# Optimization experiments

Hardware: AMD Instinct MI355X
Metric: run time of the kernel (lower is better)

Reference implementation:

```python
import jax, jax.numpy as jnp
import numpy as np

N, E, H, L, B = 200000, 800000, 128, 4, 2000  # nodes, directed edges, hidden, layers, graphs
ATOM, BOND = 28, 6


def setup_inputs() -> dict:
    key = jax.random.key(0)
    ks = jax.random.split(key, 12)
    h = jax.random.normal(ks[0], (N, ATOM), jnp.float32)
    e = jax.random.normal(ks[1], (E, BOND), jnp.float32)
    # paired directed edges: edge 2i = (u->v), edge 2i+1 = (v->u), so rev(k) = k ^ 1
    u = jax.random.randint(ks[2], (E // 2,), 0, N)
    v = jax.random.randint(ks[3], (E // 2,), 0, N)
    src = jnp.stack([u, v], axis=1).reshape(-1)
    dst = jnp.stack([v, u], axis=1).reshape(-1)
    graph_id = jnp.sort(jax.random.randint(ks[4], (N,), 0, B))
    s = 1.0 / np.sqrt(H).astype(np.float32)
    W_emb = jax.random.normal(ks[5], (ATOM, H), jnp.float32) * (1.0 / np.sqrt(ATOM))
    W_init = jax.random.normal(ks[6], (H + BOND, H), jnp.float32) * s
    b_init = jnp.zeros((H,), jnp.float32)
    W_layers = jax.random.normal(ks[7], (L, H, H), jnp.float32) * s
    b_layers = jnp.zeros((L, H), jnp.float32)
    W_ro = jax.random.normal(ks[8], (H, H), jnp.float32) * s
    W_pred = jax.random.normal(ks[9], (H, 1), jnp.float32) * s
    b_pred = jnp.zeros((1,), jnp.float32)
    snorm_n = jnp.ones((N, 1), jnp.float32)
    snorm_e = jnp.ones((E, 1), jnp.float32)
    return dict(h=h, e=e, W_emb=W_emb, W_init=W_init, b_init=b_init,
                W_layers=W_layers, b_layers=b_layers, W_ro=W_ro,
                W_pred=W_pred, b_pred=b_pred, src=src, dst=dst,
                graph_id=graph_id, snorm_n=snorm_n, snorm_e=snorm_e)


def reference(h, e, W_emb, W_init, b_init, W_layers, b_layers, W_ro,
              W_pred, b_pred, src, dst, graph_id, snorm_n, snorm_e):
    n_nodes = h.shape[0]
    n_edges = src.shape[0]
    rev = jnp.arange(n_edges) ^ 1  # paired reverse-edge index
    # node embedding (dropout is identity at p=0); x kept as residual input per source
    x = h @ W_emb  # [N, H]
    # init_message_func: per-edge relu(Linear(cat(h_src, e)))
    he = jax.nn.relu(jnp.concatenate([x[src], e], axis=1) @ W_init + b_init)  # [E, H]
    # D-MPNN layers: aggregate incoming edge states at src node, exclude reverse edge,
    # linear + relu (norms disabled in this config), outer residual add
    n_layers = W_layers.shape[0]
    for l in range(n_layers):
        agg = jax.ops.segment_sum(he, dst, num_segments=n_nodes)  # sum of edge states into each node
        m = agg[src] - he[rev]                                    # exclude reverse edge
        he = jax.nn.relu(m @ W_layers[l] + b_layers[l]) + he      # residual
    # update_all(copy_edge, sum): node state = sum of incoming edge states
    h_out = jax.ops.segment_sum(he, dst, num_segments=n_nodes)  # [N, H]
    h_ro = h_out @ W_ro                                          # linear_ro (no bias)
    # readout == 'sum': per-graph sum of node states
    hg = jax.ops.segment_sum(h_ro, graph_id, num_segments=B)     # [B, H]
    return hg @ W_pred + b_pred                                  # [B, 1]
```

## Files before the change

kernel.cpp:

```cpp
#include <hip/hip_runtime.h>
#include <hip/hip_bf16.h>

#define H 128
#define ATOM 28
#define BOND 6
#define NLAYERS 4
#define TE 32
#define LW 136
#define LKI 72
#define LE 40
typedef unsigned short US;
typedef unsigned int UI;
typedef short bf16x8 __attribute__((ext_vector_type(8)));
typedef float f32x4 __attribute__((ext_vector_type(4)));
#define MFMA(a,b,c) __builtin_amdgcn_mfma_f32_16x16x32_bf16((a),(b),(c),0,0,0)

__device__ __forceinline__ float bf2f(US u) {
    union { unsigned int i; float f; } v; v.i = ((unsigned int)u) << 16; return v.f;
}
__device__ __forceinline__ US f2bf(float f) {
    union { float f; unsigned int i; } v; v.f = f;
    unsigned int r = v.i + 0x7FFF + ((v.i >> 16) & 1);
    return (US)(r >> 16);
}
__device__ __forceinline__ float in_ld(const void* p, long long i, int bf) {
    return bf ? bf2f(((const US*)p)[i]) : ((const float*)p)[i];
}

__global__ void detect_kernel(const void* snorm, int* flag) {
    const US* u = (const US*)snorm;
    *flag = (u[0] == 0x3F80 && u[2] == 0x3F80) ? 1 : 0;
}

__global__ void fail_kernel(void* out, int nB, float val, const int* flag) {
    int i = blockIdx.x * 256 + threadIdx.x;
    if (i < nB) {
        if (*flag) ((US*)out)[i] = f2bf(val);
        else       ((float*)out)[i] = val;
    }
}

__global__ void build_wt(const void* __restrict__ W_emb, const void* __restrict__ W_init,
                         const int* __restrict__ flag, US* __restrict__ WtG) {
    int bf = *flag;
    int k = blockIdx.x;
    int c = threadIdx.x;
    float v = 0.f;
    if (k < ATOM) {
        for (int j = 0; j < H; ++j)
            v += in_ld(W_emb, k * H + j, bf) * in_ld(W_init, (long long)j * H + c, bf);
    }
    WtG[c * 64 + k] = f2bf(v);
}

__global__ void build_w2x(const void* __restrict__ W_init, const int* __restrict__ flag,
                          US* __restrict__ W2x) {
    int bf = *flag;
    int k = blockIdx.x;
    int c = threadIdx.x;
    float v = (k < BOND) ? in_ld(W_init, (long long)(H + k) * H + c, bf) : 0.f;
    W2x[c * 32 + k] = f2bf(v);
}

__global__ void build_wtL(const void* __restrict__ W_layers, const int* __restrict__ flag,
                          US* __restrict__ WtL) {
    int bf = *flag;
    int l = blockIdx.x >> 7, n = blockIdx.x & 127;
    int k = threadIdx.x;
    long long si = (long long)l * H * H + (long long)k * H + n;
    WtL[((long long)l * H + n) * H + k] = bf ? ((const US*)W_layers)[si]
                                             : f2bf(((const float*)W_layers)[si]);
}

__global__ void build_wp(const void* __restrict__ W_ro, const void* __restrict__ W_pred,
                         const int* __restrict__ flag, float* __restrict__ wp) {
    int bf = *flag;
    int c = threadIdx.x;
    float s = 0.f;
    for (int j = 0; j < H; ++j)
        s += in_ld(W_ro, (long long)c * H + j, bf) * in_ld(W_pred, j, bf);
    wp[c] = s;
}

__global__ void hist_kernel(const int* __restrict__ dst, int* __restrict__ cnt, int nE) {
    int k = blockIdx.x * 256 + threadIdx.x;
    if (k < nE) atomicAdd(&cnt[dst[k]], 1);
}

__global__ __launch_bounds__(256) void scan1(const int* __restrict__ cnt,
                                             int* __restrict__ rowptr,
                                             int* __restrict__ partials, int nN) {
    __shared__ int sd[256];
    int t = threadIdx.x;
    int base = blockIdx.x * 1024 + t * 4;
    int l0 = (base + 0 < nN) ? cnt[base + 0] : 0;
    int l1 = (base + 1 < nN) ? cnt[base + 1] : 0;
    int l2 = (base + 2 < nN) ? cnt[base + 2] : 0;
    int l3 = (base + 3 < nN) ? cnt[base + 3] : 0;
    int s = l0 + l1 + l2 + l3;
    sd[t] = s; __syncthreads();
    for (int off = 1; off < 256; off <<= 1) {
        int v = (t >= off) ? sd[t - off] : 0;
        __syncthreads();
        sd[t] += v;
        __syncthreads();
    }
    int excl = sd[t] - s;
    if (base + 0 < nN) rowptr[base + 0] = excl;
    if (base + 1 < nN) rowptr[base + 1] = excl + l0;
    if (base + 2 < nN) rowptr[base + 2] = excl + l0 + l1;
    if (base + 3 < nN) rowptr[base + 3] = excl + l0 + l1 + l2;
    if (t == 255) partials[blockIdx.x] = sd[255];
}

__global__ __launch_bounds__(256) void scan2(const int* __restrict__ partials,
                                             int* __restrict__ blockoff, int SB) {
    __shared__ int sd[256];
    int t = threadIdx.x;
    int v = (t < SB) ? partials[t] : 0;
    sd[t] = v; __syncthreads();
    for (int off = 1; off < 256; off <<= 1) {
        int x = (t >= off) ? sd[t - off] : 0;
        __syncthreads();
        sd[t] += x;
        __syncthreads();
    }
    blockoff[t] = sd[t] - v;
}

__global__ void scan3(int* __restrict__ rowptr, int* __restrict__ cursor,
                      const int* __restrict__ blockoff, int nN, int nE) {
    int i = blockIdx.x * 256 + threadIdx.x;
    if (i < nN) {
        int v = rowptr[i] + blockoff[i >> 10];
        rowptr[i] = v;
        cursor[i] = v;
    }
    if (i == 0) rowptr[nN] = nE;
}

__global__ void fill_kernel(const int* __restrict__ dst, int* __restrict__ cursor,
                            int* __restrict__ ein, int nE) {
    int k = blockIdx.x * 256 + threadIdx.x;
    if (k < nE) {
        int pos = atomicAdd(&cursor[dst[k]], 1);
        ein[pos] = k;
    }
}

__global__ __launch_bounds__(256) void agg_gather(
    const US* __restrict__ he, const int* __restrict__ rowptr,
    const int* __restrict__ ein, US* __restrict__ agg, int nN) {
    int n = blockIdx.x * 4 + (threadIdx.x >> 6);
    int lane = threadIdx.x & 63;
    if (n >= nN) return;
    const UI* heU = (const UI*)he;
    int s = rowptr[n], epos = rowptr[n + 1];
    float f0 = 0.f, f1 = 0.f;
    int idx = s;
    for (; idx + 4 <= epos; idx += 4) {
        int e0 = ein[idx], e1 = ein[idx + 1], e2 = ein[idx + 2], e3 = ein[idx + 3];
        UI u0 = heU[(long long)e0 * 64 + lane];
        UI u1 = heU[(long long)e1 * 64 + lane];
        UI u2 = heU[(long long)e2 * 64 + lane];
        UI u3 = heU[(long long)e3 * 64 + lane];
        f0 += bf2f((US)(u0 & 0xFFFF)) + bf2f((US)(u1 & 0xFFFF))
            + bf2f((US)(u2 & 0xFFFF)) + bf2f((US)(u3 & 0xFFFF));
        f1 += bf2f((US)(u0 >> 16)) + bf2f((US)(u1 >> 16))
            + bf2f((US)(u2 >> 16)) + bf2f((US)(u3 >> 16));
    }
    for (; idx < epos; ++idx) {
        UI u = heU[(long long)ein[idx] * 64 + lane];
        f0 += bf2f((US)(u & 0xFFFF));
        f1 += bf2f((US)(u >> 16));
    }
    ((UI*)agg)[(long long)n * 64 + lane] = (UI)f2bf(f0) | ((UI)f2bf(f1) << 16);
}

__global__ __launch_bounds__(256) void readout_dot(
    const US* __restrict__ he, const int* __restrict__ rowptr,
    const int* __restrict__ ein, const float* __restrict__ wp,
    const int* __restrict__ graph_id, float* __restrict__ hgS, int nN) {
    __shared__ float sv[4];
    __shared__ int sg[4];
    int wave = threadIdx.x >> 6, lane = threadIdx.x & 63;
    int n = blockIdx.x * 4 + wave;
    bool valid = n < nN;
    float w0 = wp[2 * lane], w1 = wp[2 * lane + 1];
    float v = 0.f;
    if (valid) {
        const UI* heU = (const UI*)he;
        int s = rowptr[n], epos = rowptr[n + 1];
        float f0 = 0.f, f1 = 0.f;
        int idx = s;
        for (; idx + 4 <= epos; idx += 4) {
            int e0 = ein[idx], e1 = ein[idx + 1], e2 = ein[idx + 2], e3 = ein[idx + 3];
            UI u0 = heU[(long long)e0 * 64 + lane];
            UI u1 = heU[(long long)e1 * 64 + lane];
            UI u2 = heU[(long long)e2 * 64 + lane];
            UI u3 = heU[(long long)e3 * 64 + lane];
            f0 += bf2f((US)(u0 & 0xFFFF)) + bf2f((US)(u1 & 0xFFFF))
                + bf2f((US)(u2 & 0xFFFF)) + bf2f((US)(u3 & 0xFFFF));
            f1 += bf2f((US)(u0 >> 16)) + bf2f((US)(u1 >> 16))
                + bf2f((US)(u2 >> 16)) + bf2f((US)(u3 >> 16));
        }
        for (; idx < epos; ++idx) {
            UI u = heU[(long long)ein[idx] * 64 + lane];
            f0 += bf2f((US)(u & 0xFFFF));
            f1 += bf2f((US)(u >> 16));
        }
        v = f0 * w0 + f1 * w1;
        #pragma unroll
        for (int off = 32; off > 0; off >>= 1) v += __shfl_down(v, off);
    }
    if (lane == 0) {
        sv[wave] = valid ? v : 0.f;
        sg[wave] = valid ? graph_id[n] : -1;
    }
    __syncthreads();
    if (threadIdx.x == 0) {
        int cg = sg[0]; float acc = sv[0];
        #pragma unroll
        for (int w = 1; w < 4; ++w) {
            if (sg[w] == cg) acc += sv[w];
            else {
                if (cg >= 0) unsafeAtomicAdd(&hgS[cg], acc);
                cg = sg[w]; acc = sv[w];
            }
        }
        if (cg >= 0) unsafeAtomicAdd(&hgS[cg], acc);
    }
}

__global__ __launch_bounds__(256) void agg_dot(
    const US* __restrict__ agg, const float* __restrict__ wp,
    const int* __restrict__ graph_id, float* __restrict__ hgS, int nN) {
    __shared__ float sv[4];
    __shared__ int sg[4];
    int wave = threadIdx.x >> 6, lane = threadIdx.x & 63;
    int n = blockIdx.x * 4 + wave;
    bool valid = n < nN;
    float v = 0.f;
    if (valid) {
        UI u = ((const UI*)agg)[(long long)n * 64 + lane];
        v = bf2f((US)(u & 0xFFFF)) * wp[2 * lane]
          + bf2f((US)(u >> 16)) * wp[2 * lane + 1];
        #pragma unroll
        for (int off = 32; off > 0; off >>= 1) v += __shfl_down(v, off);
    }
    if (lane == 0) {
        sv[wave] = valid ? v : 0.f;
        sg[wave] = valid ? graph_id[n] : -1;
    }
    __syncthreads();
    if (threadIdx.x == 0) {
        int cg = sg[0]; float acc = sv[0];
        #pragma unroll
        for (int w = 1; w < 4; ++w) {
            if (sg[w] == cg) acc += sv[w];
            else {
                if (cg >= 0) unsafeAtomicAdd(&hgS[cg], acc);
                cg = sg[w]; acc = sv[w];
            }
        }
        if (cg >= 0) unsafeAtomicAdd(&hgS[cg], acc);
    }
}

__global__ void finish_kernel(const float* __restrict__ hgS, const void* __restrict__ b_pred,
                              const int* __restrict__ flag, void* __restrict__ out, int nB) {
    int bf = *flag;
    int i = blockIdx.x * 256 + threadIdx.x;
    if (i < nB) {
        float r = hgS[i] + in_ld(b_pred, 0, bf);
        if (bf) ((US*)out)[i] = f2bf(r);
        else    ((float*)out)[i] = r;
    }
}

__global__ __launch_bounds__(256) void scatter_cas(
    const US* __restrict__ he, const int* __restrict__ dst,
    US* __restrict__ agg, long long totalPairs) {
    const UI* heU = (const UI*)he;
    UI* aggU = (UI*)agg;
    long long i = (long long)blockIdx.x * blockDim.x + threadIdx.x;
    long long stride = (long long)gridDim.x * blockDim.x;
    for (; i < totalPairs; i += stride) {
        int k = (int)(i >> 6);
        int jp = (int)(i & 63);
        UI pv = heU[i];
        float v0 = bf2f((US)(pv & 0xFFFF));
        float v1 = bf2f((US)(pv >> 16));
        UI* addr = aggU + (long long)dst[k] * 64 + jp;
        UI old = *addr, assumed;
        do {
            assumed = old;
            UI nv = (UI)f2bf(bf2f((US)(assumed & 0xFFFF)) + v0)
                  | ((UI)f2bf(bf2f((US)(assumed >> 16)) + v1) << 16);
            old = atomicCAS(addr, assumed, nv);
        } while (old != assumed);
    }
}

__global__ __launch_bounds__(256) void node_gemm(
    const void* __restrict__ h, const US* __restrict__ WtG,
    const int* __restrict__ flag, US* __restrict__ xn, int nN) {
    __shared__ __align__(16) US sA[TE * LKI];
    __shared__ __align__(16) US sO[TE * LW];
    const int bf = *flag;
    const int tid = threadIdx.x;
    const int wave = tid >> 6, lane = tid & 63;
    const int quad = lane >> 4, l16 = lane & 15;
    const int ncol0 = wave * 32;
    bf16x8 bw[2][2];
    #pragma unroll
    for (int i = 0; i < 2; ++i)
        #pragma unroll
        for (int c = 0; c < 2; ++c)
            bw[i][c] = *(const bf16x8*)&WtG[(ncol0 + c * 16 + l16) * 64 + i * 32 + quad * 8];

    UI* sAU = (UI*)sA;
    for (int i = tid; i < TE * (LKI / 2); i += 256) sAU[i] = 0u;

    int ntiles = (nN + TE - 1) / TE;
    for (int t = blockIdx.x; t < ntiles; t += gridDim.x) {
        int n0 = t * TE;
        __syncthreads();
        for (int i = tid; i < TE * 14; i += 256) {
            int r = i / 14, u = i % 14;
            int n = n0 + r;
            UI v = 0;
            if (n < nN) {
                if (bf) v = ((const UI*)h)[(long long)n * 14 + u];
                else {
                    const float* hF = (const float*)h + (long long)n * ATOM + 2 * u;
                    v = (UI)f2bf(hF[0]) | ((UI)f2bf(hF[1]) << 16);
                }
            }
            sAU[r * (LKI / 2) + u] = v;
        }
        __syncthreads();

        f32x4 acc00 = {0,0,0,0}, acc01 = {0,0,0,0}, acc10 = {0,0,0,0}, acc11 = {0,0,0,0};
        #pragma unroll
        for (int i = 0; i < 2; ++i) {
            int kb = i * 32 + quad * 8;
            bf16x8 a0 = *(const bf16x8*)&sA[l16 * LKI + kb];
            bf16x8 a1 = *(const bf16x8*)&sA[(l16 + 16) * LKI + kb];
            acc00 = MFMA(a0, bw[i][0], acc00);
            acc01 = MFMA(a0, bw[i][1], acc01);
            acc10 = MFMA(a1, bw[i][0], acc10);
            acc11 = MFMA(a1, bw[i][1], acc11);
        }
        #pragma unroll
        for (int mt = 0; mt < 2; ++mt)
            #pragma unroll
            for (int reg = 0; reg < 4; ++reg) {
                int row = mt * 16 + quad * 4 + reg;
                #pragma unroll
                for (int nt = 0; nt < 2; ++nt) {
                    float a = mt ? (nt ? acc11[reg] : acc10[reg])
                                 : (nt ? acc01[reg] : acc00[reg]);
                    sO[row * LW + ncol0 + nt * 16 + l16] = f2bf(a);
                }
            }
        int row2 = lane >> 1, half = lane & 1;
        int cbase = ncol0 + half * 16;
        int n = n0 + row2;
        if (n < nN) {
            uint4 o0 = *(const uint4*)&sO[row2 * LW + cbase];
            uint4 o1 = *(const uint4*)&sO[row2 * LW + cbase + 8];
            uint4* dst4 = (uint4*)(xn + (long long)n * H + cbase);
            dst4[0] = o0; dst4[1] = o1;
        }
    }
}

__global__ __launch_bounds__(256) void init_edge(
    const void* __restrict__ e, const US* __restrict__ xn,
    const US* __restrict__ W2x, const void* __restrict__ b_init,
    const int* __restrict__ src, const int* __restrict__ flag,
    US* __restrict__ he, int nE) {
    __shared__ __align__(16) US sE[TE * LE];
    __shared__ __align__(16) US sX[TE * LW];
    const int bf = *flag;
    const int tid = threadIdx.x;
    const int wave = tid >> 6, lane = tid & 63;
    const int quad = lane >> 4, l16 = lane & 15;
    const int ncol0 = wave * 32;
    float rb0 = in_ld(b_init, ncol0 + l16, bf);
    float rb1 = in_ld(b_init, ncol0 + 16 + l16, bf);
    bf16x8 bw2[2];
    #pragma unroll
    for (int c = 0; c < 2; ++c)
        bw2[c] = *(const bf16x8*)&W2x[(ncol0 + c * 16 + l16) * 32 + quad * 8];

    UI* sEU = (UI*)sE;
    for (int i = tid; i < TE * (LE / 2); i += 256) sEU[i] = 0u;

    int ntiles = nE / TE;
    for (int t = blockIdx.x; t < ntiles; t += gridDim.x) {
        int k0 = t * TE;
        __syncthreads();
        if (tid < TE * 3) {
            int r = tid / 3, u = tid % 3;
            UI v;
            if (bf) v = ((const UI*)e)[(long long)(k0 + r) * 3 + u];
            else {
                const float* eF = (const float*)e + (long long)(k0 + r) * BOND + 2 * u;
                v = (UI)f2bf(eF[0]) | ((UI)f2bf(eF[1]) << 16);
            }
            sEU[r * (LE / 2) + u] = v;
        }
        #pragma unroll
        for (int ii = 0; ii < 2; ++ii) {
            int i = tid + ii * 256;
            int r = i >> 4, q = i & 15;
            int s = src[k0 + r];
            *(uint4*)&sX[r * LW + q * 8] = ((const uint4*)(xn + (long long)s * H))[q];
        }
        __syncthreads();

        f32x4 acc00 = {0,0,0,0}, acc01 = {0,0,0,0}, acc10 = {0,0,0,0}, acc11 = {0,0,0,0};
        {
            int kb = quad * 8;
            bf16x8 a0 = *(const bf16x8*)&sE[l16 * LE + kb];
            bf16x8 a1 = *(const bf16x8*)&sE[(l16 + 16) * LE + kb];
            acc00 = MFMA(a0, bw2[0], acc00);
            acc01 = MFMA(a0, bw2[1], acc01);
            acc10 = MFMA(a1, bw2[0], acc10);
            acc11 = MFMA(a1, bw2[1], acc11);
        }
        #pragma unroll
        for (int mt = 0; mt < 2; ++mt)
            #pragma unroll
            for (int reg = 0; reg < 4; ++reg) {
                int row = mt * 16 + quad * 4 + reg;
                #pragma unroll
                for (int nt = 0; nt < 2; ++nt) {
                    float a = mt ? (nt ? acc11[reg] : acc10[reg])
                                 : (nt ? acc01[reg] : acc00[reg]);
                    int col = ncol0 + nt * 16 + l16;
                    float v = fmaxf(a + bf2f(sX[row * LW + col]) + (nt ? rb1 : rb0), 0.f);
                    sX[row * LW + col] = f2bf(v);
                }
            }
        int row2 = lane >> 1, half = lane & 1;
        int cbase = ncol0 + half * 16;
        uint4 o0 = *(const uint4*)&sX[row2 * LW + cbase];
        uint4 o1 = *(const uint4*)&sX[row2 * LW + cbase + 8];
        uint4* dst4 = (uint4*)(he + (long long)(k0 + row2) * H + cbase);
        dst4[0] = o0; dst4[1] = o1;
    }
}

__global__ __launch_bounds__(256) void mfma_layer(
    const US* __restrict__ agg, const int* __restrict__ src,
    const US* __restrict__ WtL, const void* __restrict__ b_layers,
    int layer, const int* __restrict__ flag, US* __restrict__ he, int nE) {
    __shared__ __align__(16) US sHe[2][TE * LW];
    __shared__ __align__(16) US sAgg[2][TE * LW];
    const int bf = *flag;
    const int tid = threadIdx.x;
    const int wave = tid >> 6, lane = tid & 63;
    const int quad = lane >> 4, l16 = lane & 15;
    const int ncol0 = wave * 32;
    float rb0 = in_ld(b_layers, (long long)layer * H + ncol0 + l16, bf);
    float rb1 = in_ld(b_layers, (long long)layer * H + ncol0 + 16 + l16, bf);
    const US* Wl = WtL + (size_t)layer * H * H;
    bf16x8 bw[4][2];
    #pragma unroll
    for (int i = 0; i < 4; ++i)
        #pragma unroll
        for (int c = 0; c < 2; ++c)
            bw[i][c] = *(const bf16x8*)&Wl[(ncol0 + c * 16 + l16) * H + i * 32 + quad * 8];

    const int r0 = tid >> 4, q0 = tid & 15;
    int ntiles = nE / TE;
    int t = blockIdx.x;
    uint4 vh0, vh1, va0, va1;
    if (t < ntiles) {
        int k0 = t * TE;
        const uint4* heG = (const uint4*)(he + (long long)k0 * H);
        vh0 = heG[tid]; vh1 = heG[tid + 256];
        int s0 = src[k0 + r0], s1 = src[k0 + r0 + 16];
        va0 = ((const uint4*)(agg + (long long)s0 * H))[q0];
        va1 = ((const uint4*)(agg + (long long)s1 * H))[q0];
    }
    int buf = 0;
    for (; t < ntiles; t += gridDim.x, buf ^= 1) {
        int k0 = t * TE;
        *(uint4*)&sHe[buf][r0 * LW + q0 * 8] = vh0;
        *(uint4*)&sHe[buf][(r0 + 16) * LW + q0 * 8] = vh1;
        *(uint4*)&sAgg[buf][r0 * LW + q0 * 8] = va0;
        *(uint4*)&sAgg[buf][(r0 + 16) * LW + q0 * 8] = va1;
        __syncthreads();
        int tn = t + gridDim.x;
        if (tn < ntiles) {
            int kn = tn * TE;
            const uint4* heG = (const uint4*)(he + (long long)kn * H);
            vh0 = heG[tid]; vh1 = heG[tid + 256];
            int s0 = src[kn + r0], s1 = src[kn + r0 + 16];
            va0 = ((const uint4*)(agg + (long long)s0 * H))[q0];
            va1 = ((const uint4*)(agg + (long long)s1 * H))[q0];
        }

        f32x4 g1a = {0,0,0,0}, g1b = {0,0,0,0}, g1c = {0,0,0,0}, g1d = {0,0,0,0};
        f32x4 g2a = {0,0,0,0}, g2b = {0,0,0,0}, g2c = {0,0,0,0}, g2d = {0,0,0,0};
        #pragma unroll
        for (int i = 0; i < 4; ++i) {
            int kb = i * 32 + quad * 8;
            bf16x8 aA0 = *(const bf16x8*)&sAgg[buf][l16 * LW + kb];
            bf16x8 aA1 = *(const bf16x8*)&sAgg[buf][(l16 + 16) * LW + kb];
            bf16x8 aH0 = *(const bf16x8*)&sHe[buf][l16 * LW + kb];
            bf16x8 aH1 = *(const bf16x8*)&sHe[buf][(l16 + 16) * LW + kb];
            g1a = MFMA(aA0, bw[i][0], g1a); g1b = MFMA(aA0, bw[i][1], g1b);
            g1c = MFMA(aA1, bw[i][0], g1c); g1d = MFMA(aA1, bw[i][1], g1d);
            g2a = MFMA(aH0, bw[i][0], g2a); g2b = MFMA(aH0, bw[i][1], g2b);
            g2c = MFMA(aH1, bw[i][0], g2c); g2d = MFMA(aH1, bw[i][1], g2d);
        }
        __syncthreads();

        #pragma unroll
        for (int mt = 0; mt < 2; ++mt)
            #pragma unroll
            for (int reg = 0; reg < 4; ++reg) {
                int row = mt * 16 + quad * 4 + reg;
                #pragma unroll
                for (int nt = 0; nt < 2; ++nt) {
                    float g1 = mt ? (nt ? g1d[reg] : g1c[reg])
                                  : (nt ? g1b[reg] : g1a[reg]);
                    float g2 = mt ? (nt ? g2d[reg ^ 1] : g2c[reg ^ 1])
                                  : (nt ? g2b[reg ^ 1] : g2a[reg ^ 1]);
                    int col = ncol0 + nt * 16 + l16;
                    float v = fmaxf(g1 - g2 + (nt ? rb1 : rb0), 0.f)
                            + bf2f(sHe[buf][row * LW + col]);
                    sAgg[buf][row * LW + col] = f2bf(v);
                }
            }
        int row2 = lane >> 1, half = lane & 1;
        int cbase = ncol0 + half * 16;
        uint4 o0 = *(const uint4*)&sAgg[buf][row2 * LW + cbase];
        uint4 o1 = *(const uint4*)&sAgg[buf][row2 * LW + cbase + 8];
        uint4* dst4 = (uint4*)(he + (long long)(k0 + row2) * H + cbase);
        dst4[0] = o0; dst4[1] = o1;
    }
}

extern "C" void kernel_launch(void* const* d_in, const int* in_sizes, int n_in,
                              void* d_out, int out_size, void* d_ws, size_t ws_size,
                              hipStream_t stream) {
    const void* h        = d_in[0];
    const void* e        = d_in[1];
    const void* W_emb    = d_in[2];
    const void* W_init   = d_in[3];
    const void* b_init   = d_in[4];
    const void* W_layers = d_in[5];
    const void* b_layers = d_in[6];
    const void* W_ro     = d_in[7];
    const void* W_pred   = d_in[8];
    const void* b_pred   = d_in[9];
    const int*  src      = (const int*)d_in[10];
    const int*  dst      = (const int*)d_in[11];
    const int*  graph_id = (const int*)d_in[12];
    const void* snorm_n  = d_in[13];

    int nN = in_sizes[0] / ATOM;
    int nE = in_sizes[1] / BOND;
    int nB = out_size;
    int SB = (nN + 1023) / 1024;

    size_t off = 0;
    auto alloc = [&](size_t bytes) { size_t o = off; off = (off + bytes + 255) & ~(size_t)255; return o; };
    size_t o_flag = alloc(256);
    size_t o_wt   = alloc((size_t)H * 64 * sizeof(US));
    size_t o_w2x  = alloc((size_t)H * 32 * sizeof(US));
    size_t o_wtL  = alloc((size_t)NLAYERS * H * H * sizeof(US));
    size_t o_wp   = alloc((size_t)H * sizeof(float));
    size_t o_hgs  = alloc((size_t)nB * sizeof(float));
    size_t o_cnt  = alloc((size_t)nN * sizeof(int));
    size_t o_rp   = alloc((size_t)(nN + 1) * sizeof(int));
    size_t o_cur  = alloc((size_t)nN * sizeof(int));
    size_t o_par  = alloc(256 * sizeof(int));
    size_t o_boff = alloc(256 * sizeof(int));
    size_t o_ein  = alloc((size_t)nE * sizeof(int));
    size_t o_agg  = alloc((size_t)nN * H * sizeof(US));
    size_t o_he   = alloc((size_t)nE * H * sizeof(US));
    size_t needG  = off;

    char* W = (char*)d_ws;
    int*   flag   = (int*)(W + o_flag);
    US*    WtG    = (US*)(W + o_wt);
    US*    W2x    = (US*)(W + o_w2x);
    US*    WtL    = (US*)(W + o_wtL);
    float* wp     = (float*)(W + o_wp);
    float* hgS    = (float*)(W + o_hgs);
    int*   cnt    = (int*)(W + o_cnt);
    int*   rowptr = (int*)(W + o_rp);
    int*   cursor = (int*)(W + o_cur);
    int*   part   = (int*)(W + o_par);
    int*   boff   = (int*)(W + o_boff);
    int*   ein    = (int*)(W + o_ein);
    US*    agg    = (US*)(W + o_agg);
    US*    he     = (US*)(W + o_he);

    detect_kernel<<<1, 1, 0, stream>>>(snorm_n, flag);
    build_wt<<<64, 128, 0, stream>>>(W_emb, W_init, flag, WtG);
    build_w2x<<<32, 128, 0, stream>>>(W_init, flag, W2x);
    build_wtL<<<NLAYERS * H, 128, 0, stream>>>(W_layers, flag, WtL);
    build_wp<<<1, 128, 0, stream>>>(W_ro, W_pred, flag, wp);

    if (ws_size >= needG && SB <= 256) {
        hipMemsetAsync(cnt, 0, (size_t)nN * sizeof(int), stream);
        hist_kernel<<<(nE + 255) / 256, 256, 0, stream>>>(dst, cnt, nE);
        scan1<<<SB, 256, 0, stream>>>(cnt, rowptr, part, nN);
        scan2<<<1, 256, 0, stream>>>(part, boff, SB);
        scan3<<<(nN + 255) / 256, 256, 0, stream>>>(rowptr, cursor, boff, nN, nE);
        fill_kernel<<<(nE + 255) / 256, 256, 0, stream>>>(dst, cursor, ein, nE);

        node_gemm<<<2048, 256, 0, stream>>>(h, WtG, flag, agg , nN);
        init_edge<<<2048, 256, 0, stream>>>(e, agg , W2x, b_init, src, flag, he, nE);
        for (int l = 0; l < NLAYERS; ++l) {
            agg_gather<<<(nN + 3) / 4, 256, 0, stream>>>(he, rowptr, ein, agg, nN);
            mfma_layer<<<2048, 256, 0, stream>>>(agg, src, WtL, b_layers, l, flag, he, nE);
        }
        hipMemsetAsync(hgS, 0, (size_t)nB * sizeof(float), stream);
        readout_dot<<<(nN + 3) / 4, 256, 0, stream>>>(he, rowptr, ein, wp, graph_id, hgS, nN);
        finish_kernel<<<(nB + 255) / 256, 256, 0, stream>>>(hgS, b_pred, flag, d_out, nB);
        return;
    }

    size_t off2 = 0;
    auto alloc2 = [&](size_t bytes) { size_t o = off2; off2 = (off2 + bytes + 255) & ~(size_t)255; return o; };
    alloc2(256);
    alloc2((size_t)H * 64 * sizeof(US));
    alloc2((size_t)H * 32 * sizeof(US));
    alloc2((size_t)NLAYERS * H * H * sizeof(US));
    size_t f2_wp  = alloc2((size_t)H * sizeof(float));
    size_t f2_hgs = alloc2((size_t)nB * sizeof(float));
    size_t f2_agg = alloc2((size_t)nN * H * sizeof(US));
    size_t f2_he  = alloc2((size_t)nE * H * sizeof(US));
    size_t needT  = off2;

    if (ws_size >= needT) {
        float* wp2  = (float*)(W + f2_wp);
        float* hgS2 = (float*)(W + f2_hgs);
        US*    agg2 = (US*)(W + f2_agg);
        US*    he2  = (US*)(W + f2_he);
        build_wp<<<1, 128, 0, stream>>>(W_ro, W_pred, flag, wp2);
        node_gemm<<<2048, 256, 0, stream>>>(h, WtG, flag, agg2 , nN);
        init_edge<<<2048, 256, 0, stream>>>(e, agg2, W2x, b_init, src, flag, he2, nE);
        for (int l = 0; l < NLAYERS; ++l) {
            hipMemsetAsync(agg2, 0, (size_t)nN * H * sizeof(US), stream);
            scatter_cas<<<2048, 256, 0, stream>>>(he2, dst, agg2, (long long)nE * (H / 2));
            mfma_layer<<<2048, 256, 0, stream>>>(agg2, src, WtL, b_layers, l, flag, he2, nE);
        }
        hipMemsetAsync(agg2, 0, (size_t)nN * H * sizeof(US), stream);
        scatter_cas<<<2048, 256, 0, stream>>>(he2, dst, agg2, (long long)nE * (H / 2));
        hipMemsetAsync(hgS2, 0, (size_t)nB * sizeof(float), stream);
        agg_dot<<<(nN + 3) / 4, 256, 0, stream>>>(agg2, wp2, graph_id, hgS2, nN);
        finish_kernel<<<(nB + 255) / 256, 256, 0, stream>>>(hgS2, b_pred, flag, d_out, nB);
    } else {
        float val = (float)(ws_size >> 20) * 1e6f;
        fail_kernel<<<(nB + 255) / 256, 256, 0, stream>>>(d_out, nB, val, flag);
    }
}
```

Before: 1.124 ms.

## Stream edge readout dot then node gather; double-buffer init_edge loads

The fused readout, which gathered edge states per node and then took a dot product, becomes two kernels. The first computes a per-edge scalar dot with the folded readout weight, streaming the edge-state matrix in order. The second gathers only those scalars per node and does the per-graph segmented atomic reduction. Separately, init_edge now prefetches the next tile's edge features and source node rows into registers and double-buffers its shared memory, so gather latency overlaps the MFMA work. This adds a per-edge float buffer and an extra launch.

```diff
diff --git a/kernel.cpp b/kernel.cpp
--- a/kernel.cpp
+++ b/kernel.cpp
@@ -177,58 +177,66 @@
     ((UI*)agg)[(long long)n * 64 + lane] = (UI)f2bf(f0) | ((UI)f2bf(f1) << 16);
 }
 
-__global__ __launch_bounds__(256) void readout_dot(
-    const US* __restrict__ he, const int* __restrict__ rowptr,
-    const int* __restrict__ ein, const float* __restrict__ wp,
-    const int* __restrict__ graph_id, float* __restrict__ hgS, int nN) {
-    __shared__ float sv[4];
-    __shared__ int sg[4];
-    int wave = threadIdx.x >> 6, lane = threadIdx.x & 63;
-    int n = blockIdx.x * 4 + wave;
-    bool valid = n < nN;
+__global__ __launch_bounds__(256) void edge_dot(
+    const US* __restrict__ he, const float* __restrict__ wp,
+    float* __restrict__ s, int nE) {
+    int wave = (int)((blockIdx.x * blockDim.x + threadIdx.x) >> 6);
+    int lane = threadIdx.x & 63;
+    int k0 = wave * 4;
+    if (k0 >= nE) return;
+    const UI* heU = (const UI*)he;
     float w0 = wp[2 * lane], w1 = wp[2 * lane + 1];
-    float v = 0.f;
-    if (valid) {
-        const UI* heU = (const UI*)he;
-        int s = rowptr[n], epos = rowptr[n + 1];
-        float f0 = 0.f, f1 = 0.f;
-        int idx = s;
-        for (; idx + 4 <= epos; idx += 4) {
-            int e0 = ein[idx], e1 = ein[idx + 1], e2 = ein[idx + 2], e3 = ein[idx + 3];
-            UI u0 = heU[(long long)e0 * 64 + lane];
-            UI u1 = heU[(long long)e1 * 64 + lane];
-            UI u2 = heU[(long long)e2 * 64 + lane];
-            UI u3 = heU[(long long)e3 * 64 + lane];
-            f0 += bf2f((US)(u0 & 0xFFFF)) + bf2f((US)(u1 & 0xFFFF))
-                + bf2f((US)(u2 & 0xFFFF)) + bf2f((US)(u3 & 0xFFFF));
-            f1 += bf2f((US)(u0 >> 16)) + bf2f((US)(u1 >> 16))
-                + bf2f((US)(u2 >> 16)) + bf2f((US)(u3 >> 16));
-        }
-        for (; idx < epos; ++idx) {
-            UI u = heU[(long long)ein[idx] * 64 + lane];
-            f0 += bf2f((US)(u & 0xFFFF));
-            f1 += bf2f((US)(u >> 16));
-        }
-        v = f0 * w0 + f1 * w1;
-        #pragma unroll
-        for (int off = 32; off > 0; off >>= 1) v += __shfl_down(v, off);
-    }
-    if (lane == 0) {
-        sv[wave] = valid ? v : 0.f;
-        sg[wave] = valid ? graph_id[n] : -1;
-    }
+    float d0, d1, d2, d3;
+    {
+        UI u0 = heU[(long long)k0 * 64 + lane];
+        UI u1 = heU[(long long)(k0 + 1) * 64 + lane];
+        UI u2 = heU[(long long)(k0 + 2) * 64 + lane];
+        UI u3 = heU[(long long)(k0 + 3) * 64 + lane];
+        d0 = bf2f((US)(u0 & 0xFFFF)) * w0 + bf2f((US)(u0 >> 16)) * w1;
+        d1 = bf2f((US)(u1 & 0xFFFF)) * w0 + bf2f((US)(u1 >> 16)) * w1;
+        d2 = bf2f((US)(u2 & 0xFFFF)) * w0 + bf2f((US)(u2 >> 16)) * w1;
+        d3 = bf2f((US)(u3 & 0xFFFF)) * w0 + bf2f((US)(u3 >> 16)) * w1;
+    }
+    #pragma unroll
+    for (int off = 1; off < 64; off <<= 1) {
+        d0 += __shfl_xor(d0, off);
+        d1 += __shfl_xor(d1, off);
+        d2 += __shfl_xor(d2, off);
+        d3 += __shfl_xor(d3, off);
+    }
+    if (lane < 4) {
+        float v = (lane == 0) ? d0 : (lane == 1) ? d1 : (lane == 2) ? d2 : d3;
+        s[k0 + lane] = v;
+    }
+}
+
+__global__ __launch_bounds__(256) void node_sum(
+    const float* __restrict__ s, const int* __restrict__ rowptr,
+    const int* __restrict__ ein, const int* __restrict__ graph_id,
+    float* __restrict__ hgS, int nN) {
+    __shared__ int sg[256];
+    __shared__ float sv[256];
+    int tid = threadIdx.x;
+    int n = blockIdx.x * 256 + tid;
+    float acc = 0.f;
+    int g = -1;
+    if (n < nN) {
+        g = graph_id[n];
+        int e0 = rowptr[n], e1 = rowptr[n + 1];
+        for (int idx = e0; idx < e1; ++idx) acc += s[ein[idx]];
+    }
+    sg[tid] = g; sv[tid] = acc;
     __syncthreads();
-    if (threadIdx.x == 0) {
-        int cg = sg[0]; float acc = sv[0];
-        #pragma unroll
-        for (int w = 1; w < 4; ++w) {
-            if (sg[w] == cg) acc += sv[w];
+    if (tid == 0) {
+        int cg = sg[0]; float a = sv[0];
+        for (int i = 1; i < 256; ++i) {
+            if (sg[i] == cg) a += sv[i];
             else {
-                if (cg >= 0) unsafeAtomicAdd(&hgS[cg], acc);
-                cg = sg[w]; acc = sv[w];
-            }
-        }
-        if (cg >= 0) unsafeAtomicAdd(&hgS[cg], acc);
+                if (cg >= 0) unsafeAtomicAdd(&hgS[cg], a);
+                cg = sg[i]; a = sv[i];
+            }
+        }
+        if (cg >= 0) unsafeAtomicAdd(&hgS[cg], a);
     }
 }
 
@@ -381,8 +389,8 @@
     const US* __restrict__ W2x, const void* __restrict__ b_init,
     const int* __restrict__ src, const int* __restrict__ flag,
     US* __restrict__ he, int nE) {
-    __shared__ __align__(16) US sE[TE * LE];
-    __shared__ __align__(16) US sX[TE * LW];
+    __shared__ __align__(16) US sE[2][TE * LE];
+    __shared__ __align__(16) US sX[2][TE * LW];
     const int bf = *flag;
     const int tid = threadIdx.x;
     const int wave = tid >> 6, lane = tid & 63;
@@ -395,37 +403,56 @@
     for (int c = 0; c < 2; ++c)
         bw2[c] = *(const bf16x8*)&W2x[(ncol0 + c * 16 + l16) * 32 + quad * 8];
 
-    UI* sEU = (UI*)sE;
-    for (int i = tid; i < TE * (LE / 2); i += 256) sEU[i] = 0u;
-
+    for (int b = 0; b < 2; ++b) {
+        UI* z = (UI*)sE[b];
+        for (int i = tid; i < TE * (LE / 2); i += 256) z[i] = 0u;
+    }
+
+    const int r0 = tid >> 4, q0 = tid & 15;
+    const int er = tid / 3, eu = tid - er * 3;
     int ntiles = nE / TE;
-    for (int t = blockIdx.x; t < ntiles; t += gridDim.x) {
+    int t = blockIdx.x;
+    UI ve = 0; uint4 vx0, vx1;
+    if (t < ntiles) {
         int k0 = t * TE;
-        __syncthreads();
-        if (tid < TE * 3) {
-            int r = tid / 3, u = tid % 3;
-            UI v;
-            if (bf) v = ((const UI*)e)[(long long)(k0 + r) * 3 + u];
+        if (tid < 96) {
+            if (bf) ve = ((const UI*)e)[(long long)(k0 + er) * 3 + eu];
             else {
-                const float* eF = (const float*)e + (long long)(k0 + r) * BOND + 2 * u;
-                v = (UI)f2bf(eF[0]) | ((UI)f2bf(eF[1]) << 16);
-            }
-            sEU[r * (LE / 2) + u] = v;
-        }
-        #pragma unroll
-        for (int ii = 0; ii < 2; ++ii) {
-            int i = tid + ii * 256;
-            int r = i >> 4, q = i & 15;
-            int s = src[k0 + r];
-            *(uint4*)&sX[r * LW + q * 8] = ((const uint4*)(xn + (long long)s * H))[q];
-        }
-        __syncthreads();
+                const float* eF = (const float*)e + (long long)(k0 + er) * BOND + 2 * eu;
+                ve = (UI)f2bf(eF[0]) | ((UI)f2bf(eF[1]) << 16);
+            }
+        }
+        int s0 = src[k0 + r0], s1 = src[k0 + r0 + 16];
+        vx0 = ((const uint4*)(xn + (long long)s0 * H))[q0];
+        vx1 = ((const uint4*)(xn + (long long)s1 * H))[q0];
+    }
+    int buf = 0;
+    for (; t < ntiles; t += gridDim.x, buf ^= 1) {
+        int k0 = t * TE;
+        if (tid < 96) ((UI*)sE[buf])[er * (LE / 2) + eu] = ve;
+        *(uint4*)&sX[buf][r0 * LW + q0 * 8] = vx0;
+        *(uint4*)&sX[buf][(r0 + 16) * LW + q0 * 8] = vx1;
+        __syncthreads();
+        int tn = t + gridDim.x;
+        if (tn < ntiles) {
+            int kn = tn * TE;
+            if (tid < 96) {
+                if (bf) ve = ((const UI*)e)[(long long)(kn + er) * 3 + eu];
+                else {
+                    const float* eF = (const float*)e + (long long)(kn + er) * BOND + 2 * eu;
+                    ve = (UI)f2bf(eF[0]) | ((UI)f2bf(eF[1]) << 16);
+                }
+            }
+            int s0 = src[kn + r0], s1 = src[kn + r0 + 16];
+            vx0 = ((const uint4*)(xn + (long long)s0 * H))[q0];
+            vx1 = ((const uint4*)(xn + (long long)s1 * H))[q0];
+        }
 
         f32x4 acc00 = {0,0,0,0}, acc01 = {0,0,0,0}, acc10 = {0,0,0,0}, acc11 = {0,0,0,0};
         {
             int kb = quad * 8;
-            bf16x8 a0 = *(const bf16x8*)&sE[l16 * LE + kb];
-            bf16x8 a1 = *(const bf16x8*)&sE[(l16 + 16) * LE + kb];
+            bf16x8 a0 = *(const bf16x8*)&sE[buf][l16 * LE + kb];
+            bf16x8 a1 = *(const bf16x8*)&sE[buf][(l16 + 16) * LE + kb];
             acc00 = MFMA(a0, bw2[0], acc00);
             acc01 = MFMA(a0, bw2[1], acc01);
             acc10 = MFMA(a1, bw2[0], acc10);
@@ -441,14 +468,14 @@
                     float a = mt ? (nt ? acc11[reg] : acc10[reg])
                                  : (nt ? acc01[reg] : acc00[reg]);
                     int col = ncol0 + nt * 16 + l16;
-                    float v = fmaxf(a + bf2f(sX[row * LW + col]) + (nt ? rb1 : rb0), 0.f);
-                    sX[row * LW + col] = f2bf(v);
+                    float v = fmaxf(a + bf2f(sX[buf][row * LW + col]) + (nt ? rb1 : rb0), 0.f);
+                    sX[buf][row * LW + col] = f2bf(v);
                 }
             }
         int row2 = lane >> 1, half = lane & 1;
         int cbase = ncol0 + half * 16;
-        uint4 o0 = *(const uint4*)&sX[row2 * LW + cbase];
-        uint4 o1 = *(const uint4*)&sX[row2 * LW + cbase + 8];
+        uint4 o0 = *(const uint4*)&sX[buf][row2 * LW + cbase];
+        uint4 o1 = *(const uint4*)&sX[buf][row2 * LW + cbase + 8];
         uint4* dst4 = (uint4*)(he + (long long)(k0 + row2) * H + cbase);
         dst4[0] = o0; dst4[1] = o1;
     }
@@ -584,6 +611,7 @@
     size_t o_par  = alloc(256 * sizeof(int));
     size_t o_boff = alloc(256 * sizeof(int));
     size_t o_ein  = alloc((size_t)nE * sizeof(int));
+    size_t o_s    = alloc((size_t)nE * sizeof(float));
     size_t o_agg  = alloc((size_t)nN * H * sizeof(US));
     size_t o_he   = alloc((size_t)nE * H * sizeof(US));
     size_t needG  = off;
@@ -601,6 +629,7 @@
     int*   part   = (int*)(W + o_par);
     int*   boff   = (int*)(W + o_boff);
     int*   ein    = (int*)(W + o_ein);
+    float* sbuf   = (float*)(W + o_s);
     US*    agg    = (US*)(W + o_agg);
     US*    he     = (US*)(W + o_he);
 
@@ -625,7 +654,8 @@
             mfma_layer<<<2048, 256, 0, stream>>>(agg, src, WtL, b_layers, l, flag, he, nE);
         }
         hipMemsetAsync(hgS, 0, (size_t)nB * sizeof(float), stream);
-        readout_dot<<<(nN + 3) / 4, 256, 0, stream>>>(he, rowptr, ein, wp, graph_id, hgS, nN);
+        edge_dot<<<(nE + 15) / 16, 256, 0, stream>>>(he, wp, sbuf, nE);
+        node_sum<<<(nN + 255) / 256, 256, 0, stream>>>(sbuf, rowptr, ein, graph_id, hgS, nN);
         finish_kernel<<<(nB + 255) / 256, 256, 0, stream>>>(hgS, b_pred, flag, d_out, nB);
         return;
     }
```

New measurement: 1.121 ms. Within noise of the previous version (-0.2%).
